# Performance work log

Measured on AMD Instinct MI355X. Metric: run time of the kernel, lower is better.

## Reference

```python
import jax, jax.numpy as jnp
import numpy as np

NUM_LAYERS = 4
D_MODEL = 1024
N_HEAD = 8
HEAD_DIM = D_MODEL // N_HEAD
FFN_DIM = 4096
B, L = 8, 512
LN_EPS = 1e-5


def rel_pos_embed(seq_len, dim, init_size=1200, padding_idx=0):
    # RelativeSinusoidalPositionalEmbedding.get_embedding(init_size+1, dim, 0)
    num = init_size + 1  # 1201
    half = dim // 2
    inv = np.exp(np.arange(half, dtype=np.float64) * -(np.log(10000.0) / (half - 1)))
    pos = np.arange(-num // 2, num // 2, dtype=np.float64)[:, None] * inv[None, :]
    emb = np.concatenate([np.sin(pos), np.cos(pos)], axis=1)  # [num, dim]
    emb[padding_idx] = 0.0
    origin_shift = num // 2 + 1  # 601
    idx = np.arange(-seq_len, seq_len) + origin_shift  # [2L]
    return jnp.asarray(emb[idx], dtype=jnp.float32)  # [2L, dim]


def _shift(BD):
    # [b,h,L,2L] -> [b,h,L,L], selecting relative offsets k-q
    b, h, l, _ = BD.shape
    BD = jnp.concatenate([BD, jnp.zeros((b, h, l, 1), BD.dtype)], axis=-1)
    BD = BD.reshape(b, h, -1, l)[:, :, :-1].reshape(b, h, l, 2 * l)
    return BD[:, :, :, l:]


def _transpose_shift(E):
    # [b,h,L,2L] -> [b,h,L,L]
    b, h, l, _ = E.shape
    E = jnp.concatenate([E, jnp.zeros((b, h, l, 1), E.dtype)], axis=-1)
    E = E.reshape(b, h, 2 * l + 1, l)
    E = E[:, :, 2 * jnp.arange(l) + 1, :]  # [b,h,L,L]
    return jnp.swapaxes(E, -1, -2)


def layer_norm(x, g, b):
    mu = x.mean(-1, keepdims=True)
    var = ((x - mu) ** 2).mean(-1, keepdims=True)
    return (x - mu) / jnp.sqrt(var + LN_EPS) * g + b


def rel_attn(x, mask, qkv_w, r_r, r_w, pos):
    bsz, l, d = x.shape
    qkv = x @ qkv_w  # [b,L,3D]
    q, k, v = jnp.split(qkv, 3, axis=-1)
    to_heads = lambda t: t.reshape(bsz, l, N_HEAD, HEAD_DIM).transpose(0, 2, 1, 3)
    q, k, v = to_heads(q), to_heads(k), to_heads(v)  # [b,h,L,hd]
    rw_q = q + r_r[:, None]  # (original adds r_r_bias here)
    AC = jnp.einsum('bnqd,bnkd->bnqk', rw_q, k)
    D_ = jnp.einsum('nd,ld->nl', r_w, pos)[None, :, None]   # [1,h,1,2L]
    B_ = jnp.einsum('bnqd,ld->bnql', q, pos)                # [b,h,L,2L]
    E_ = jnp.einsum('bnqd,ld->bnql', k, pos)
    BDE = _shift(B_ + D_) + _transpose_shift(E_)
    attn = AC + BDE  # scale == 1 (scale=False)
    attn = jnp.where(mask[:, None, None, :] == 0, -jnp.inf, attn)
    attn = jax.nn.softmax(attn, axis=-1)
    out = jnp.einsum('bnqk,bnkd->bnqd', attn, v)
    return out.transpose(0, 2, 1, 3).reshape(bsz, l, d)


def setup_inputs() -> dict:
    key = jax.random.key(0)
    ks = jax.random.split(key, 12)
    Ln = NUM_LAYERS
    s = 0.02
    return {
        'x': jax.random.normal(ks[0], (B, L, D_MODEL), jnp.float32),
        'mask': jnp.ones((B, L), jnp.int32),
        'qkv_w': jax.random.normal(ks[1], (Ln, D_MODEL, 3 * D_MODEL), jnp.float32) * s,
        'r_r_bias': jax.random.normal(ks[2], (Ln, N_HEAD, HEAD_DIM), jnp.float32) * s,
        'r_w_bias': jax.random.normal(ks[3], (Ln, N_HEAD, HEAD_DIM), jnp.float32) * s,
        'ln1_g': jnp.ones((Ln, D_MODEL), jnp.float32),
        'ln1_b': jnp.zeros((Ln, D_MODEL), jnp.float32),
        'ln2_g': jnp.ones((Ln, D_MODEL), jnp.float32),
        'ln2_b': jnp.zeros((Ln, D_MODEL), jnp.float32),
        'w1': jax.random.normal(ks[4], (Ln, D_MODEL, FFN_DIM), jnp.float32) * s,
        'b1': jnp.zeros((Ln, FFN_DIM), jnp.float32),
        'w2': jax.random.normal(ks[5], (Ln, FFN_DIM, D_MODEL), jnp.float32) * s,
        'b2': jnp.zeros((Ln, D_MODEL), jnp.float32),
    }


def reference(x, mask, qkv_w, r_r_bias, r_w_bias, ln1_g, ln1_b, ln2_g, ln2_b, w1, b1, w2, b2):
    pos = rel_pos_embed(x.shape[1], HEAD_DIM)  # [2L, hd], buffer (detached)
    for i in range(NUM_LAYERS):  # after_norm=True (post-LN)
        a = rel_attn(x, mask, qkv_w[i], r_r_bias[i], r_w_bias[i], pos)
        x = layer_norm(x + a, ln1_g[i], ln1_b[i])
        h = jax.nn.relu(x @ w1[i] + b1[i]) @ w2[i] + b2[i]
        x = layer_norm(x + h, ln2_g[i], ln2_b[i])
    return x
```

## Files before the change

### kernel.cpp

```cpp
#include <hip/hip_runtime.h>

#define SEQ 512
#define DM 1024
#define NH 8
#define HD 128
#define FFN 4096
#define NL 4
#define NB 8

typedef __attribute__((ext_vector_type(8))) _Float16 half8v;
typedef __attribute__((ext_vector_type(8))) unsigned short ushort8v;
typedef __attribute__((ext_vector_type(4))) float float4v;

__device__ __forceinline__ unsigned short f2h(float f) {
  _Float16 h = (_Float16)f;
  return *(unsigned short*)&h;
}
__device__ __forceinline__ float h2f(unsigned short u) {
  _Float16 h = *(_Float16*)&u;
  return (float)h;
}

__global__ void sc_kernel(float* __restrict__ sc) {
  int idx = blockIdx.x * blockDim.x + threadIdx.x;
  int q = idx >> 6, c = idx & 63;
  if (q >= SEQ) return;
  double a = exp(-(double)c * (9.210340371976184 / 63.0));
  double p = (double)q * a;
  sc[q * 128 + c] = (float)sin(p);
  sc[q * 128 + 64 + c] = (float)cos(p);
}

__global__ void cvt_copy(const float* __restrict__ in, float* __restrict__ xout,
                         unsigned short* __restrict__ xh, int n4) {
  int i = blockIdx.x * blockDim.x + threadIdx.x;
  if (i >= n4) return;
  float4 v = ((const float4*)in)[i];
  ((float4*)xout)[i] = v;
  ushort4 u;
  u.x = f2h(v.x); u.y = f2h(v.y); u.z = f2h(v.z); u.w = f2h(v.w);
  ((ushort4*)xh)[i] = u;
}

__global__ __launch_bounds__(256) void transpose_cvt(
    const float* __restrict__ in, unsigned short* __restrict__ out, int K, int N) {
  __shared__ float t[32][33];
  int n0 = blockIdx.x * 32, k0 = blockIdx.y * 32;
  int c = threadIdx.x & 31, r = threadIdx.x >> 5;
#pragma unroll
  for (int i = 0; i < 32; i += 8)
    t[r + i][c] = in[(long long)(k0 + r + i) * N + n0 + c];
  __syncthreads();
#pragma unroll
  for (int i = 0; i < 32; i += 8)
    out[(long long)(n0 + r + i) * K + k0 + c] = f2h(t[c][r + i]);
}

template<int R, int T>
__device__ __forceinline__ void stage_tile(
    const unsigned short* __restrict__ g, long long ld, int k0,
    unsigned short* lds, int tid) {
#pragma unroll
  for (int i = 0; i < R * 64 / 8 / T; i++) {
    int p = i * T + tid;
    int row = p >> 3, cs = p & 7;
    int c = cs ^ (row & 7);
    const unsigned short* src = g + (long long)row * ld + k0 + c * 8;
    __builtin_amdgcn_global_load_lds(
        (const __attribute__((address_space(1))) void*)src,
        (__attribute__((address_space(3))) void*)(lds + p * 8),
        16, 0, 0);
  }
}

__device__ __forceinline__ void load_stage128(
    const unsigned short* __restrict__ g, long long ld, int k0, int tid, ushort8v* v) {
#pragma unroll
  for (int i = 0; i < 2; i++) {
    int p = i * 512 + tid;
    int row = p >> 3, cs = p & 7;
    int c = cs ^ (row & 7);
    v[i] = *(const ushort8v*)(g + (long long)row * ld + k0 + c * 8);
  }
}
__device__ __forceinline__ void write_stage128(
    unsigned short* St, int tid, const ushort8v* v) {
#pragma unroll
  for (int i = 0; i < 2; i++)
    *(ushort8v*)(St + (i * 512 + tid) * 8) = v[i];
}

template<int BIAS, int RELU, int OUTH>
__global__ __launch_bounds__(512, 2) void gemm256(
    const unsigned short* __restrict__ A, int lda, long long sAz,
    const unsigned short* __restrict__ Bt, int ldb, long long sBz,
    const float* __restrict__ bias,
    void* __restrict__ Cv, int ldc, long long sCz,
    int K) {
  __shared__ __align__(16) unsigned short As[2][256 * 64];
  __shared__ __align__(16) unsigned short Bs[2][256 * 64];
  const int tid = threadIdx.x, lane = tid & 63, w = tid >> 6;
  const int wm = w >> 2, wn = w & 3;
  const int l15 = lane & 15, l4 = lane >> 4;
  const int gx = gridDim.x, gy = gridDim.y;
  int nwg = gx * gy * gridDim.z;
  int lin = (blockIdx.z * gy + blockIdx.y) * gx + blockIdx.x;
  int swz = (lin & 7) * (nwg >> 3) + (lin >> 3);
  int bx = swz % gx;
  int t2 = swz / gx;
  int by = t2 % gy;
  int z  = t2 / gy;
  const unsigned short* Ag = A + (long long)z * sAz + (long long)by * 256 * lda;
  const unsigned short* Bg = Bt + (long long)z * sBz + (long long)bx * 256 * ldb;

  float4v acc[8][4] = {};
  const int nt = K >> 6;
  stage_tile<256, 512>(Ag, lda, 0, As[0], tid);
  stage_tile<256, 512>(Bg, ldb, 0, Bs[0], tid);
  int cur = 0;
  for (int t = 0; t < nt; t++) {
    if (t + 1 < nt) {
      stage_tile<256, 512>(Ag, lda, (t + 1) << 6, As[cur ^ 1], tid);
      stage_tile<256, 512>(Bg, ldb, (t + 1) << 6, Bs[cur ^ 1], tid);
      asm volatile("s_waitcnt vmcnt(8)" ::: "memory");
    } else {
      asm volatile("s_waitcnt vmcnt(0)" ::: "memory");
    }
    asm volatile("s_barrier" ::: "memory");
#pragma unroll
    for (int ks = 0; ks < 2; ks++) {
      half8v af[8], bf[4];
#pragma unroll
      for (int m = 0; m < 8; m++) {
        int row = wm * 128 + m * 16 + l15;
        int cs = (ks * 4 + l4) ^ (row & 7);
        af[m] = *(const half8v*)&As[cur][row * 64 + cs * 8];
      }
#pragma unroll
      for (int n = 0; n < 4; n++) {
        int row = wn * 64 + n * 16 + l15;
        int cs = (ks * 4 + l4) ^ (row & 7);
        bf[n] = *(const half8v*)&Bs[cur][row * 64 + cs * 8];
      }
#pragma unroll
      for (int m = 0; m < 8; m++)
#pragma unroll
        for (int n = 0; n < 4; n++)
          acc[m][n] = __builtin_amdgcn_mfma_f32_16x16x32_f16(af[m], bf[n], acc[m][n], 0, 0, 0);
    }
    asm volatile("s_barrier" ::: "memory");
    cur ^= 1;
  }
#pragma unroll
  for (int n = 0; n < 4; n++) {
    int ccol = bx * 256 + wn * 64 + n * 16 + l15;
    float bv = BIAS ? bias[ccol] : 0.f;
#pragma unroll
    for (int m = 0; m < 8; m++) {
      int crow0 = by * 256 + wm * 128 + m * 16 + l4 * 4;
#pragma unroll
      for (int j = 0; j < 4; j++) {
        float v = acc[m][n][j] + bv;
        if (RELU) v = fmaxf(v, 0.f);
        long long off = (long long)z * sCz + (long long)(crow0 + j) * ldc + ccol;
        if (OUTH) ((unsigned short*)Cv)[off] = f2h(v);
        else      ((float*)Cv)[off] = v;
      }
    }
  }
}

__global__ __launch_bounds__(256) void build_aug(
    const unsigned short* __restrict__ qkv_h,
    const float* __restrict__ rr, const float* __restrict__ rw,
    const float* __restrict__ sc,
    unsigned short* __restrict__ Ahat, unsigned short* __restrict__ Bhat)
{
  const int z = blockIdx.y, b = z >> 3, h = z & 7;
  const int r = threadIdx.x >> 7, lane = threadIdx.x & 127;
  const int q = blockIdx.x * 2 + r;
  __shared__ float Qf[2][128], Kf[2][128], SC[2][128];
  const unsigned short* row = qkv_h + ((long long)(b * SEQ + q)) * 3072 + h * HD;
  float qv = h2f(row[lane]);
  float kv = h2f(row[DM + lane]);
  Qf[r][lane] = qv + rw[h * HD + lane];
  Kf[r][lane] = kv;
  SC[r][lane] = sc[q * 128 + lane];
  __syncthreads();
  unsigned short* Arow = Ahat + ((long long)z * SEQ + q) * 384;
  unsigned short* Brow = Bhat + ((long long)z * SEQ + q) * 384;
  Arow[lane] = f2h(qv + rr[h * HD + lane]);
  Brow[lane] = f2h(kv);
  if (lane < 64) {
    float S = SC[r][lane], C = SC[r][64 + lane];
    Arow[128 + lane] = f2h(Qf[r][lane] * C + Qf[r][64 + lane] * S);
    Arow[256 + lane] = f2h(S);
    Brow[128 + lane] = f2h(S);
    Brow[256 + lane] = f2h(Kf[r][lane] * C + Kf[r][64 + lane] * S);
  } else {
    int c = lane - 64;
    float S = SC[r][c], C = SC[r][lane];
    Arow[192 + c] = f2h(Qf[r][lane] * C - Qf[r][c] * S);
    Arow[320 + c] = f2h(C);
    Brow[192 + c] = f2h(C);
    Brow[320 + c] = f2h(Kf[r][lane] * C - Kf[r][c] * S);
  }
}

__global__ __launch_bounds__(256) void transpose_v(
    const unsigned short* __restrict__ qkv_h, unsigned short* __restrict__ Vt)
{
  __shared__ unsigned short t[32][33];
  const int z = blockIdx.z, b = z >> 3, h = z & 7;
  const int d0 = blockIdx.x * 32, j0 = blockIdx.y * 32;
  const int c = threadIdx.x & 31, r = threadIdx.x >> 5;
#pragma unroll
  for (int i = 0; i < 32; i += 8)
    t[r + i][c] = qkv_h[((long long)(b * SEQ + j0 + r + i)) * 3072 + 2 * DM + h * HD + d0 + c];
  __syncthreads();
#pragma unroll
  for (int i = 0; i < 32; i += 8)
    Vt[(long long)z * HD * SEQ + (long long)(d0 + r + i) * SEQ + j0 + c] = t[c][r + i];
}

__global__ __launch_bounds__(512, 4) void attn_fused(
    const unsigned short* __restrict__ Ahat,
    const unsigned short* __restrict__ Bhat,
    const unsigned short* __restrict__ Vt,
    const int* __restrict__ mask,
    unsigned short* __restrict__ out)
{
  __shared__ __align__(16) unsigned short S[64 * 512];
  __shared__ __align__(16) unsigned short St[128 * 64];
  const int tid = threadIdx.x, lane = tid & 63, w = tid >> 6;
  const int wr = w >> 1, wc = w & 1;
  const int l15 = lane & 15, l4 = lane >> 4;
  int lin = blockIdx.z * gridDim.x + blockIdx.x;
  int nwg = gridDim.x * gridDim.z;
  int swz = (lin & 7) * (nwg >> 3) + (lin >> 3);
  int qt = swz % gridDim.x, z = swz / gridDim.x;
  const int b = z >> 3, h = z & 7;
  const int q0 = qt * 64;

  half8v qf[12];
  {
    const unsigned short* Ar = Ahat + ((long long)z * SEQ + q0 + wr * 16 + l15) * 384;
#pragma unroll
    for (int k = 0; k < 12; k++)
      qf[k] = *(const half8v*)&Ar[k * 32 + l4 * 8];
  }

  ushort8v stg[2];
  load_stage128(Bhat + ((long long)z * SEQ) * 384, 384, 0, tid, stg);
#pragma unroll
  for (int jt = 0; jt < 4; jt++) {
    float4v acc[4] = {};
#pragma unroll
    for (int k6 = 0; k6 < 6; k6++) {
      __builtin_amdgcn_s_barrier();
      write_stage128(St, tid, stg);
      int ns = jt * 6 + k6 + 1;
      if (ns < 24) {
        const unsigned short* Bg = Bhat + ((long long)z * SEQ + (ns / 6) * 128) * 384;
        load_stage128(Bg, 384, (ns % 6) * 64, tid, stg);
      }
      asm volatile("s_waitcnt lgkmcnt(0)" ::: "memory");
      __builtin_amdgcn_s_barrier();
      __builtin_amdgcn_s_setprio(1);
#pragma unroll
      for (int kk = 0; kk < 2; kk++) {
        int kidx = k6 * 2 + kk;
#pragma unroll
        for (int n = 0; n < 4; n++) {
          int row = wc * 64 + n * 16 + l15;
          int cs = (kk * 4 + l4) ^ (row & 7);
          half8v bf = *(const half8v*)&St[row * 64 + cs * 8];
          acc[n] = __builtin_amdgcn_mfma_f32_16x16x32_f16(qf[kidx], bf, acc[n], 0, 0, 0);
        }
      }
      __builtin_amdgcn_s_setprio(0);
    }
#pragma unroll
    for (int n = 0; n < 4; n++) {
      int col = jt * 128 + wc * 64 + n * 16 + l15;
#pragma unroll
      for (int j = 0; j < 4; j++) {
        int row = wr * 16 + l4 * 4 + j;
        int byte = (row * 512 + col) * 2;
        byte ^= (row & 7) << 4;
        *(unsigned short*)((char*)S + byte) = f2h(acc[n][j]);
      }
    }
  }

  const unsigned short* Vg = Vt + (long long)z * HD * SEQ;
  load_stage128(Vg, 512, 0, tid, stg);

  asm volatile("s_waitcnt lgkmcnt(0)" ::: "memory");
  __builtin_amdgcn_s_barrier();

  float* bias = (float*)St;
  float* Linv = (float*)St + 512;
  if (tid < 128) {
    int4 mk = ((const int4*)(mask + (size_t)b * SEQ))[tid];
    float4 bv;
    bv.x = mk.x ? 0.f : -1e30f;
    bv.y = mk.y ? 0.f : -1e30f;
    bv.z = mk.z ? 0.f : -1e30f;
    bv.w = mk.w ? 0.f : -1e30f;
    ((float4*)bias)[tid] = bv;
  }
  asm volatile("s_waitcnt lgkmcnt(0)" ::: "memory");
  __builtin_amdgcn_s_barrier();
  {
    const int row = tid >> 3;
    const int c8 = tid & 7;
    float mx = -1e30f;
#pragma unroll
    for (int i = 0; i < 8; i++) {
      int col = i * 64 + c8 * 8;
      int byte = (row * 512 + col) * 2;
      byte ^= (row & 7) << 4;
      ushort8v u = *(const ushort8v*)((const char*)S + byte);
      const float* bp = bias + col;
#pragma unroll
      for (int e = 0; e < 8; e++)
        mx = fmaxf(mx, h2f(u[e]) + bp[e]);
    }
    mx = fmaxf(mx, __shfl_xor(mx, 1));
    mx = fmaxf(mx, __shfl_xor(mx, 2));
    mx = fmaxf(mx, __shfl_xor(mx, 4));
    float sum = 0.f;
#pragma unroll
    for (int i = 0; i < 8; i++) {
      int col = i * 64 + c8 * 8;
      int byte = (row * 512 + col) * 2;
      byte ^= (row & 7) << 4;
      ushort8v u = *(const ushort8v*)((const char*)S + byte);
      const float* bp = bias + col;
#pragma unroll
      for (int e = 0; e < 8; e++) {
        float ev = __expf(h2f(u[e]) + bp[e] - mx);
        sum += ev;
        u[e] = f2h(ev);
      }
      *(ushort8v*)((char*)S + byte) = u;
    }
    sum += __shfl_xor(sum, 1);
    sum += __shfl_xor(sum, 2);
    sum += __shfl_xor(sum, 4);
    if (c8 == 0) Linv[row] = 1.f / sum;
  }
  asm volatile("s_waitcnt lgkmcnt(0)" ::: "memory");
  __builtin_amdgcn_s_barrier();
  float rs[4];
#pragma unroll
  for (int j = 0; j < 4; j++) rs[j] = Linv[wr * 16 + l4 * 4 + j];
  asm volatile("s_waitcnt lgkmcnt(0)" ::: "memory");

  float4v oacc[4] = {};
#pragma unroll
  for (int k8 = 0; k8 < 8; k8++) {
    __builtin_amdgcn_s_barrier();
    write_stage128(St, tid, stg);
    if (k8 + 1 < 8) load_stage128(Vg, 512, (k8 + 1) * 64, tid, stg);
    asm volatile("s_waitcnt lgkmcnt(0)" ::: "memory");
    __builtin_amdgcn_s_barrier();
    __builtin_amdgcn_s_setprio(1);
#pragma unroll
    for (int kk = 0; kk < 2; kk++) {
      int prow = wr * 16 + l15;
      int pb = (prow * 512 + k8 * 64 + kk * 32 + l4 * 8) * 2;
      pb ^= (prow & 7) << 4;
      half8v af = *(const half8v*)((const char*)S + pb);
#pragma unroll
      for (int n = 0; n < 4; n++) {
        int row = wc * 64 + n * 16 + l15;
        int cs = (kk * 4 + l4) ^ (row & 7);
        half8v bf = *(const half8v*)&St[row * 64 + cs * 8];
        oacc[n] = __builtin_amdgcn_mfma_f32_16x16x32_f16(af, bf, oacc[n], 0, 0, 0);
      }
    }
    __builtin_amdgcn_s_setprio(0);
  }
#pragma unroll
  for (int j = 0; j < 4; j++) {
    int row = q0 + wr * 16 + l4 * 4 + j;
#pragma unroll
    for (int n = 0; n < 4; n++) {
      int col = h * HD + wc * 64 + n * 16 + l15;
      out[((long long)(b * SEQ + row)) * DM + col] = f2h(oacc[n][j] * rs[j]);
    }
  }
}

__global__ __launch_bounds__(256) void add_ln_cvt(
    float* __restrict__ x, const unsigned short* __restrict__ a,
    const float* __restrict__ g, const float* __restrict__ bt,
    unsigned short* __restrict__ xh)
{
  const int row = blockIdx.x, tid = threadIdx.x;
  float4* xp = (float4*)(x + (size_t)row * DM);
  const ushort4 av = ((const ushort4*)(a + (size_t)row * DM))[tid];
  float4 xv = xp[tid];
  float4 s = make_float4(xv.x + h2f(av.x), xv.y + h2f(av.y),
                         xv.z + h2f(av.z), xv.w + h2f(av.w));
  __shared__ float red[4];
  float sum = s.x + s.y + s.z + s.w;
  for (int o = 32; o; o >>= 1) sum += __shfl_down(sum, o);
  if ((tid & 63) == 0) red[tid >> 6] = sum;
  __syncthreads();
  float mu = (red[0] + red[1] + red[2] + red[3]) * (1.f / DM);
  float dx = s.x - mu, dy = s.y - mu, dz = s.z - mu, dw = s.w - mu;
  float sq = dx * dx + dy * dy + dz * dz + dw * dw;
  for (int o = 32; o; o >>= 1) sq += __shfl_down(sq, o);
  __syncthreads();
  if ((tid & 63) == 0) red[tid >> 6] = sq;
  __syncthreads();
  float var = (red[0] + red[1] + red[2] + red[3]) * (1.f / DM);
  float rstd = rsqrtf(var + 1e-5f);
  const float4 gv = ((const float4*)g)[tid];
  const float4 bv = ((const float4*)bt)[tid];
  float4 o4 = make_float4(dx * rstd * gv.x + bv.x, dy * rstd * gv.y + bv.y,
                          dz * rstd * gv.z + bv.z, dw * rstd * gv.w + bv.w);
  xp[tid] = o4;
  ushort4 u;
  u.x = f2h(o4.x); u.y = f2h(o4.y); u.z = f2h(o4.z); u.w = f2h(o4.w);
  ((ushort4*)(xh + (size_t)row * DM))[tid] = u;
}

__global__ __launch_bounds__(256) void add_ln_cvt4(
    float* __restrict__ x, const unsigned short* __restrict__ p, long long pstride,
    const float* __restrict__ bias,
    const float* __restrict__ g, const float* __restrict__ bt,
    unsigned short* __restrict__ xh)
{
  const int row = blockIdx.x, tid = threadIdx.x;
  float4* xp = (float4*)(x + (size_t)row * DM);
  const float4 bb = ((const float4*)bias)[tid];
  float4 xv = xp[tid];
  float4 s = make_float4(xv.x + bb.x, xv.y + bb.y, xv.z + bb.z, xv.w + bb.w);
#pragma unroll
  for (int zz = 0; zz < 4; zz++) {
    const ushort4 a = ((const ushort4*)(p + zz * pstride + (size_t)row * DM))[tid];
    s.x += h2f(a.x); s.y += h2f(a.y); s.z += h2f(a.z); s.w += h2f(a.w);
  }
  __shared__ float red[4];
  float sum = s.x + s.y + s.z + s.w;
  for (int o = 32; o; o >>= 1) sum += __shfl_down(sum, o);
  if ((tid & 63) == 0) red[tid >> 6] = sum;
  __syncthreads();
  float mu = (red[0] + red[1] + red[2] + red[3]) * (1.f / DM);
  float dx = s.x - mu, dy = s.y - mu, dz = s.z - mu, dw = s.w - mu;
  float sq = dx * dx + dy * dy + dz * dz + dw * dw;
  for (int o = 32; o; o >>= 1) sq += __shfl_down(sq, o);
  __syncthreads();
  if ((tid & 63) == 0) red[tid >> 6] = sq;
  __syncthreads();
  float var = (red[0] + red[1] + red[2] + red[3]) * (1.f / DM);
  float rstd = rsqrtf(var + 1e-5f);
  const float4 gv = ((const float4*)g)[tid];
  const float4 bv = ((const float4*)bt)[tid];
  float4 o4 = make_float4(dx * rstd * gv.x + bv.x, dy * rstd * gv.y + bv.y,
                          dz * rstd * gv.z + bv.z, dw * rstd * gv.w + bv.w);
  xp[tid] = o4;
  ushort4 u;
  u.x = f2h(o4.x); u.y = f2h(o4.y); u.z = f2h(o4.z); u.w = f2h(o4.w);
  ((ushort4*)(xh + (size_t)row * DM))[tid] = u;
}

extern "C" void kernel_launch(void* const* d_in, const int* in_sizes, int n_in,
                              void* d_out, int out_size, void* d_ws, size_t ws_size,
                              hipStream_t stream)
{
  const float* x_in = (const float*)d_in[0];
  const int*   mask = (const int*)d_in[1];
  const float* qkv_w = (const float*)d_in[2];
  const float* r_r  = (const float*)d_in[3];
  const float* r_w  = (const float*)d_in[4];
  const float* ln1g = (const float*)d_in[5];
  const float* ln1b = (const float*)d_in[6];
  const float* ln2g = (const float*)d_in[7];
  const float* ln2b = (const float*)d_in[8];
  const float* w1   = (const float*)d_in[9];
  const float* b1   = (const float*)d_in[10];
  const float* w2   = (const float*)d_in[11];
  const float* b2   = (const float*)d_in[12];
  float* x = (float*)d_out;
  char* ws = (char*)d_ws;

  const int ROWS = NB * SEQ;

  const size_t sc_off   = 0;
  const size_t xh_off   = 0x40000;
  const size_t wt_off   = xh_off + (size_t)ROWS * DM * 2;
  const size_t a16_off  = wt_off + (size_t)FFN * DM * 2;
  const size_t qkvh_off = a16_off + (size_t)ROWS * DM * 2;
  const size_t e_off    = qkvh_off + (size_t)ROWS * 3 * DM * 2;

  const size_t ab_bytes = (size_t)64 * SEQ * 384 * 2;
  const size_t hb_bytes = (size_t)ROWS * FFN * 2;
  const size_t part_off = e_off + hb_bytes;

  float* sc     = (float*)(ws + sc_off);
  unsigned short* xh = (unsigned short*)(ws + xh_off);
  unsigned short* wt = (unsigned short*)(ws + wt_off);
  unsigned short* a16 = (unsigned short*)(ws + a16_off);
  unsigned short* qkvh = (unsigned short*)(ws + qkvh_off);
  unsigned short* Ahat = (unsigned short*)(ws + e_off);
  unsigned short* Bhat = (unsigned short*)(ws + e_off + ab_bytes);
  unsigned short* Vt   = (unsigned short*)(ws + e_off + 2 * ab_bytes);
  unsigned short* hb = (unsigned short*)(ws + e_off);
  unsigned short* part = (unsigned short*)(ws + part_off);

  sc_kernel<<<dim3(SEQ * 64 / 256), 256, 0, stream>>>(sc);
  cvt_copy<<<dim3(ROWS * DM / 4 / 256), 256, 0, stream>>>(x_in, x, xh, ROWS * DM / 4);

  for (int L = 0; L < NL; L++) {
    transpose_cvt<<<dim3(3 * DM / 32, DM / 32), 256, 0, stream>>>(
        qkv_w + (size_t)L * DM * 3 * DM, wt, DM, 3 * DM);
    gemm256<0,0,1><<<dim3(3 * DM / 256, ROWS / 256, 1), 512, 0, stream>>>(
        xh, DM, 0, wt, DM, 0, nullptr, qkvh, 3 * DM, 0, DM);

    build_aug<<<dim3(SEQ / 2, 64), 256, 0, stream>>>(
        qkvh, r_r + (size_t)L * NH * HD, r_w + (size_t)L * NH * HD, sc, Ahat, Bhat);
    transpose_v<<<dim3(HD / 32, SEQ / 32, 64), 256, 0, stream>>>(qkvh, Vt);
    attn_fused<<<dim3(SEQ / 64, 1, 64), 512, 0, stream>>>(Ahat, Bhat, Vt, mask, a16);

    add_ln_cvt<<<dim3(ROWS), 256, 0, stream>>>(x, a16, ln1g + (size_t)L * DM, ln1b + (size_t)L * DM, xh);

    transpose_cvt<<<dim3(FFN / 32, DM / 32), 256, 0, stream>>>(
        w1 + (size_t)L * DM * FFN, wt, DM, FFN);
    gemm256<1,1,1><<<dim3(FFN / 256, ROWS / 256, 1), 512, 0, stream>>>(
        xh, DM, 0, wt, DM, 0, b1 + (size_t)L * FFN, hb, FFN, 0, DM);

    transpose_cvt<<<dim3(DM / 32, FFN / 32), 256, 0, stream>>>(
        w2 + (size_t)L * FFN * DM, wt, FFN, DM);
    gemm256<0,0,1><<<dim3(DM / 256, ROWS / 256, 4), 512, 0, stream>>>(
        hb, FFN, 1024, wt, FFN, 1024, nullptr,
        part, DM, (long long)ROWS * DM, 1024);

    add_ln_cvt4<<<dim3(ROWS), 256, 0, stream>>>(
        x, part, (long long)ROWS * DM, b2 + (size_t)L * DM,
        ln2g + (size_t)L * DM, ln2b + (size_t)L * DM, xh);
  }
}
```

Before: 863.9 us.

## Interleave GEMM prefetch chunks with MFMA phases and raise wave priority

The main GEMM loop is split into four phases per K-tile. Each phase issues one chunk of the next tile's global-to-LDS loads, then runs its share of MFMAs under s_setprio(1), with barriers between phases. This spreads memory traffic across the compute instead of issuing it all up front, and halves the B-fragment registers held at once. In exchange it adds more barriers per iteration and reloads B fragments, and the vmcnt accounting has to match the chunked issue order.

```diff
diff --git a/kernel.cpp b/kernel.cpp
--- a/kernel.cpp
+++ b/kernel.cpp
@@ -71,6 +71,19 @@
         (__attribute__((address_space(3))) void*)(lds + p * 8),
         16, 0, 0);
   }
+}
+
+__device__ __forceinline__ void stage_chunk(
+    const unsigned short* __restrict__ g, long long ld, int k0,
+    unsigned short* lds, int tid, int i) {
+  int p = i * 512 + tid;
+  int row = p >> 3, cs = p & 7;
+  int c = cs ^ (row & 7);
+  const unsigned short* src = g + (long long)row * ld + k0 + c * 8;
+  __builtin_amdgcn_global_load_lds(
+      (const __attribute__((address_space(1))) void*)src,
+      (__attribute__((address_space(3))) void*)(lds + p * 8),
+      16, 0, 0);
 }
 
 __device__ __forceinline__ void load_stage128(
@@ -119,36 +132,66 @@
   stage_tile<256, 512>(Bg, ldb, 0, Bs[0], tid);
   int cur = 0;
   for (int t = 0; t < nt; t++) {
-    if (t + 1 < nt) {
-      stage_tile<256, 512>(Ag, lda, (t + 1) << 6, As[cur ^ 1], tid);
-      stage_tile<256, 512>(Bg, ldb, (t + 1) << 6, Bs[cur ^ 1], tid);
-      asm volatile("s_waitcnt vmcnt(8)" ::: "memory");
-    } else {
-      asm volatile("s_waitcnt vmcnt(0)" ::: "memory");
-    }
-    asm volatile("s_barrier" ::: "memory");
+    const unsigned short* Ac = As[cur];
+    const unsigned short* Bc = Bs[cur];
+    unsigned short* An = As[cur ^ 1];
+    unsigned short* Bn = Bs[cur ^ 1];
+    const int pf = (t + 1 < nt);
+    const int k1 = (t + 1) << 6;
+    half8v af[8], bf[2];
 #pragma unroll
     for (int ks = 0; ks < 2; ks++) {
-      half8v af[8], bf[4];
-#pragma unroll
-      for (int m = 0; m < 8; m++) {
-        int row = wm * 128 + m * 16 + l15;
-        int cs = (ks * 4 + l4) ^ (row & 7);
-        af[m] = *(const half8v*)&As[cur][row * 64 + cs * 8];
-      }
-#pragma unroll
-      for (int n = 0; n < 4; n++) {
-        int row = wn * 64 + n * 16 + l15;
-        int cs = (ks * 4 + l4) ^ (row & 7);
-        bf[n] = *(const half8v*)&Bs[cur][row * 64 + cs * 8];
-      }
-#pragma unroll
-      for (int m = 0; m < 8; m++)
-#pragma unroll
-        for (int n = 0; n < 4; n++)
-          acc[m][n] = __builtin_amdgcn_mfma_f32_16x16x32_f16(af[m], bf[n], acc[m][n], 0, 0, 0);
-    }
-    asm volatile("s_barrier" ::: "memory");
+#pragma unroll
+      for (int half = 0; half < 2; half++) {
+        if (ks == 0 && half == 0) {
+          if (pf) {
+            stage_chunk(Ag, lda, k1, An, tid, 0);
+            stage_chunk(Bg, ldb, k1, Bn, tid, 0);
+            asm volatile("s_waitcnt vmcnt(2)" ::: "memory");
+          } else {
+            asm volatile("s_waitcnt vmcnt(0)" ::: "memory");
+          }
+          __builtin_amdgcn_s_barrier();
+        }
+        if (half == 0) {
+#pragma unroll
+          for (int m = 0; m < 8; m++) {
+            int row = wm * 128 + m * 16 + l15;
+            int cs = (ks * 4 + l4) ^ (row & 7);
+            af[m] = *(const half8v*)&Ac[row * 64 + cs * 8];
+          }
+#pragma unroll
+          for (int n = 0; n < 2; n++) {
+            int row = wn * 64 + n * 16 + l15;
+            int cs = (ks * 4 + l4) ^ (row & 7);
+            bf[n] = *(const half8v*)&Bc[row * 64 + cs * 8];
+          }
+        } else {
+#pragma unroll
+          for (int n = 0; n < 2; n++) {
+            int row = wn * 64 + (2 + n) * 16 + l15;
+            int cs = (ks * 4 + l4) ^ (row & 7);
+            bf[n] = *(const half8v*)&Bc[row * 64 + cs * 8];
+          }
+        }
+        int p = ks * 2 + half;
+        if (pf && p > 0) {
+          stage_chunk(Ag, lda, k1, An, tid, p);
+          stage_chunk(Bg, ldb, k1, Bn, tid, p);
+        }
+        asm volatile("s_waitcnt lgkmcnt(0)" ::: "memory");
+        __builtin_amdgcn_sched_barrier(0);
+        __builtin_amdgcn_s_setprio(1);
+#pragma unroll
+        for (int m = 0; m < 8; m++)
+#pragma unroll
+          for (int n = 0; n < 2; n++)
+            acc[m][half * 2 + n] =
+                __builtin_amdgcn_mfma_f32_16x16x32_f16(af[m], bf[n], acc[m][half * 2 + n], 0, 0, 0);
+        __builtin_amdgcn_s_setprio(0);
+        __builtin_amdgcn_s_barrier();
+      }
+    }
     cur ^= 1;
   }
 #pragma unroll
```

After: 884.8 us. 1.02x slower.
